# Performance work log

Hardware: AMD Instinct MI355X
Metric: run time of the kernel (lower is better)

The kernel has to match this reference:

```python
import jax, jax.numpy as jnp
import numpy as np

DIM = 1024
HEADS = 16
DH = DIM // HEADS  # 64
DFF = 4096
EPS = 1e-5


def layer_norm(x, g, b):
    mu = jnp.mean(x, axis=-1, keepdims=True)
    var = jnp.mean(jnp.square(x - mu), axis=-1, keepdims=True)
    return (x - mu) * jax.lax.rsqrt(var + EPS) * g + b


def setup_inputs() -> dict:
    key = jax.random.key(0)
    ks = jax.random.split(key, 12)
    s = 0.02
    return {
        "encoder_input": jax.random.normal(ks[0], (4, 2048, DIM), jnp.float32),
        # per-head Q/K/V projections stacked over heads: [H, dim, d_head]
        "wq": jax.random.normal(ks[1], (HEADS, DIM, DH), jnp.float32) * s,
        "bq": jnp.zeros((HEADS, DH), jnp.float32),
        "wk": jax.random.normal(ks[2], (HEADS, DIM, DH), jnp.float32) * s,
        "bk": jnp.zeros((HEADS, DH), jnp.float32),
        "wv": jax.random.normal(ks[3], (HEADS, DIM, DH), jnp.float32) * s,
        "bv": jnp.zeros((HEADS, DH), jnp.float32),
        "ln1_g": jnp.ones((DIM,), jnp.float32),
        "ln1_b": jnp.zeros((DIM,), jnp.float32),
        "w1": jax.random.normal(ks[4], (DIM, DFF), jnp.float32) * s,
        "b1": jnp.zeros((DFF,), jnp.float32),
        "w2": jax.random.normal(ks[5], (DFF, DIM), jnp.float32) * s,
        "b2": jnp.zeros((DIM,), jnp.float32),
        "ln2_g": jnp.ones((DIM,), jnp.float32),
        "ln2_b": jnp.zeros((DIM,), jnp.float32),
    }


def reference(encoder_input, wq, bq, wk, bk, wv, bv, ln1_g, ln1_b,
              w1, b1, w2, b2, ln2_g, ln2_b):
    x = encoder_input  # [B, S, D]
    B, S, D = x.shape
    # per-head projections, batched over heads (same math as the head loop)
    q = jnp.einsum('bsd,hde->bhse', x, wq) + bq[None, :, None, :]
    k = jnp.einsum('bsd,hde->bhse', x, wk) + bk[None, :, None, :]
    v = jnp.einsum('bsd,hde->bhse', x, wv) + bv[None, :, None, :]
    scores = jnp.einsum('bhse,bhte->bhst', q, k) / jnp.sqrt(jnp.float32(DH))
    attn = jax.nn.softmax(scores, axis=-1)
    o = jnp.einsum('bhst,bhte->bhse', attn, v)  # [B, H, S, dh]
    self_attn = jnp.transpose(o, (0, 2, 1, 3)).reshape(B, S, D)  # concat heads on dim=2
    # residual: source + LayerNorm(target)  (dropout = identity in eval)
    res1 = x + layer_norm(self_attn, ln1_g, ln1_b)
    ff = jax.nn.relu(res1 @ w1 + b1) @ w2 + b2
    return res1 + layer_norm(ff, ln2_g, ln2_b)
```

## Files before the change

kernel.cpp:

```cpp
#include <hip/hip_runtime.h>
#include <cstdint>
#include <cmath>

typedef unsigned short u16;
using bf16x8 = __attribute__((ext_vector_type(8))) __bf16;
using f32x4  = __attribute__((ext_vector_type(4))) float;

#define MFMA(a, b, c) __builtin_amdgcn_mfma_f32_16x16x32_bf16((a), (b), (c), 0, 0, 0)

__device__ __forceinline__ float b2f(u16 u) {
    union { unsigned int i; float f; } x; x.i = ((unsigned int)u) << 16; return x.f;
}
__device__ __forceinline__ u16 f2b(float f) {
    union { float f; unsigned int i; } x; x.f = f;
    unsigned int r = x.i + 0x7FFFu + ((x.i >> 16) & 1u);
    return (u16)(r >> 16);
}
__device__ __forceinline__ u16 cvtb(float f) {
    __bf16 h = (__bf16)f;
    return *reinterpret_cast<u16*>(&h);
}
__device__ __forceinline__ uint32_t cvtpk(float lo, float hi) {
    uint32_t r;
    asm("v_cvt_pk_bf16_f32 %0, %1, %2" : "=v"(r) : "v"(lo), "v"(hi));
    return r;
}

__device__ __forceinline__ void gload16(const u16* g, u16* l) {
    __builtin_amdgcn_global_load_lds(
        (const __attribute__((address_space(1))) void*)g,
        (__attribute__((address_space(3))) void*)l, 16, 0, 0);
}

#define BAR do { asm volatile("" ::: "memory"); \
                 __builtin_amdgcn_s_barrier();  \
                 asm volatile("" ::: "memory"); } while (0)

#define QSCALE (0.125f * 1.44269504f)

__global__ __launch_bounds__(256) void xcvt_kernel(const float* __restrict__ X,
                                                   u16* __restrict__ Xb)
{
    size_t i = ((size_t)blockIdx.x * 256 + threadIdx.x) * 8;
    float4 a = *reinterpret_cast<const float4*>(&X[i]);
    float4 b = *reinterpret_cast<const float4*>(&X[i + 4]);
    ushort4 lo = {f2b(a.x), f2b(a.y), f2b(a.z), f2b(a.w)};
    ushort4 hi = {f2b(b.x), f2b(b.y), f2b(b.z), f2b(b.w)};
    *reinterpret_cast<ushort4*>(&Xb[i]) = lo;
    *reinterpret_cast<ushort4*>(&Xb[i + 4]) = hi;
}

__global__ __launch_bounds__(256) void wT_kernel(const float* __restrict__ W,
                                                 u16* __restrict__ Wt, int K, int N)
{
    __shared__ __align__(16) u16 Ts[64][72];
    const int k0 = blockIdx.x * 64, n0 = blockIdx.y * 64;
    const int tid = threadIdx.x;
    #pragma unroll
    for (int it = 0; it < 4; ++it) {
        int vI = tid + it * 256;
        int kr = vI >> 4, nc = (vI & 15) * 4;
        float4 f = *reinterpret_cast<const float4*>(&W[(size_t)(k0 + kr) * N + n0 + nc]);
        Ts[nc + 0][kr] = f2b(f.x);
        Ts[nc + 1][kr] = f2b(f.y);
        Ts[nc + 2][kr] = f2b(f.z);
        Ts[nc + 3][kr] = f2b(f.w);
    }
    __syncthreads();
    #pragma unroll
    for (int it = 0; it < 2; ++it) {
        int vI = tid + it * 256;
        int nr = vI >> 3, kc = (vI & 7) * 8;
        *reinterpret_cast<uint4*>(&Wt[(size_t)(n0 + nr) * K + k0 + kc]) =
            *reinterpret_cast<uint4*>(&Ts[nr][kc]);
    }
}

__global__ __launch_bounds__(256) void wqkvT_kernel(
    const float* __restrict__ Wq, const float* __restrict__ Wk,
    const float* __restrict__ Wv, u16* __restrict__ Wt)
{
    __shared__ __align__(16) u16 Ts[64][72];
    const int k0 = blockIdx.x * 64, h = blockIdx.y, m = blockIdx.z;
    const float* W = (m == 0 ? Wq : (m == 1 ? Wk : Wv)) + (size_t)h * 65536;
    const float scl = (m == 0) ? QSCALE : 1.0f;
    const int tid = threadIdx.x;
    #pragma unroll
    for (int it = 0; it < 4; ++it) {
        int vI = tid + it * 256;
        int kr = vI >> 4, dc = (vI & 15) * 4;
        float4 f = *reinterpret_cast<const float4*>(&W[(size_t)(k0 + kr) * 64 + dc]);
        Ts[dc + 0][kr] = f2b(f.x * scl);
        Ts[dc + 1][kr] = f2b(f.y * scl);
        Ts[dc + 2][kr] = f2b(f.z * scl);
        Ts[dc + 3][kr] = f2b(f.w * scl);
    }
    __syncthreads();
    #pragma unroll
    for (int it = 0; it < 2; ++it) {
        int vI = tid + it * 256;
        int dr = vI >> 3, kc = (vI & 7) * 8;
        *reinterpret_cast<uint4*>(
            &Wt[((size_t)(m * 1024 + h * 64 + dr)) * 1024 + k0 + kc]) =
            *reinterpret_cast<uint4*>(&Ts[dr][kc]);
    }
}

__global__ __launch_bounds__(256) void biascat_kernel(
    const float* __restrict__ Bq, const float* __restrict__ Bk,
    const float* __restrict__ Bv, float* __restrict__ out)
{
    int i = blockIdx.x * 256 + threadIdx.x;
    const float* B = (i < 1024 ? Bq : (i < 2048 ? Bk : Bv));
    float v = B[i & 1023];
    if (i < 1024) v *= QSCALE;
    out[i] = v;
}

__device__ __forceinline__ void stage_half(const u16* __restrict__ gb, int K,
                                           u16* lr, int lane, int w)
{
    #pragma unroll
    for (int cc = 0; cc < 2; ++cc) {
        int c = w * 2 + cc;
        int l = c * 64 + lane;
        int lp = l ^ ((l >> 3) & 7);
        gload16(gb + (size_t)(lp >> 3) * K + (lp & 7) * 8, lr + c * 512);
    }
}

template <int RELU, int F32OUT>
__global__ __launch_bounds__(512, 2) void gemm8(
    const u16* __restrict__ A, const u16* __restrict__ Bt,
    const float* __restrict__ bias, void* __restrict__ Cv,
    int M, int N, int K)
{
    __shared__ __align__(16) u16 lds[65536];
    const int tid = threadIdx.x, lane = tid & 63, w = tid >> 6;
    const int wm = w >> 2, wn = w & 3;
    const int g = lane >> 4, ln = lane & 15;
    const int xr = (ln & 7) << 3;
    const int brow = (wn & 1) * 64;

    int nwg = gridDim.x * gridDim.y;
    int bid = blockIdx.y * gridDim.x + blockIdx.x;
    int swz = (bid & 7) * (nwg >> 3) + (bid >> 3);
    const int m0 = (swz % gridDim.x) * 256;
    const int n0 = (swz / gridDim.x) * 256;

    const u16* Ab = A + (size_t)m0 * K;
    const u16* Bb = Bt + (size_t)n0 * K;

    u16* ldsA[2] = { lds + wm * 8192,         lds + 32768 + wm * 8192 };
    u16* ldsB[2] = { lds + 16384 + (wn >> 1) * 8192,
                     lds + 49152 + (wn >> 1) * 8192 };

    f32x4 acc[8][4];
    #pragma unroll
    for (int i = 0; i < 8; ++i)
        #pragma unroll
        for (int j = 0; j < 4; ++j) acc[i][j] = (f32x4){0.f, 0.f, 0.f, 0.f};

    bf16x8 af[4][2], bf[2][2];

#define RD_A(d, mh)                                                           \
    _Pragma("unroll") for (int i = 0; i < 4; ++i)                             \
    _Pragma("unroll") for (int kk = 0; kk < 2; ++kk)                          \
        af[i][kk] = *(const bf16x8*)&ldsA[d][((mh)*64 + i*16 + ln)*64 +       \
                                             ((kk*32 + g*8) ^ xr)];
#define RD_B(d, nh)                                                           \
    _Pragma("unroll") for (int j = 0; j < 2; ++j)                             \
    _Pragma("unroll") for (int kk = 0; kk < 2; ++kk)                          \
        bf[j][kk] = *(const bf16x8*)&ldsB[d][(brow + (nh)*32 + j*16 + ln)*64  \
                                             + ((kk*32 + g*8) ^ xr)];
#define MMQ(mh, nh)                                                           \
    __builtin_amdgcn_s_setprio(1);                                            \
    _Pragma("unroll") for (int i = 0; i < 4; ++i)                             \
    _Pragma("unroll") for (int j = 0; j < 2; ++j) {                           \
        acc[(mh)*4+i][(nh)*2+j] =                                             \
            MFMA(af[i][0], bf[j][0], acc[(mh)*4+i][(nh)*2+j]);                \
        acc[(mh)*4+i][(nh)*2+j] =                                             \
            MFMA(af[i][1], bf[j][1], acc[(mh)*4+i][(nh)*2+j]);                \
    }                                                                         \
    __builtin_amdgcn_s_setprio(0);

    const int ntk = K >> 6;
    const int nit = ntk >> 1;

    stage_half(Ab,                           K, lds + 0,     lane, w);
    stage_half(Ab + (size_t)128 * K,         K, lds + 8192,  lane, w);
    stage_half(Bb,                           K, lds + 16384, lane, w);
    stage_half(Bb + (size_t)128 * K,         K, lds + 24576, lane, w);
    stage_half(Ab + 64,                      K, lds + 32768, lane, w);
    stage_half(Ab + (size_t)128 * K + 64,    K, lds + 40960, lane, w);
    asm volatile("s_waitcnt vmcnt(4)" ::: "memory");
    BAR;

    for (int u = 0; u < nit; ++u) {
        const int t1 = 2 * u + 1;
        int s0 = 2 * u + 2; if (s0 >= ntk) s0 = ntk - 1;
        int s1 = 2 * u + 3; if (s1 >= ntk) s1 = ntk - 1;
        RD_A(0, 0); RD_B(0, 0);
        stage_half(Bb + (size_t)t1 * 64, K, lds + 49152, lane, w);
        BAR; MMQ(0, 0); BAR;
        RD_B(0, 1);
        stage_half(Bb + (size_t)128 * K + (size_t)t1 * 64, K, lds + 57344, lane, w);
        BAR; MMQ(0, 1); BAR;
        RD_A(0, 1); RD_B(0, 0);
        BAR; MMQ(1, 0); BAR;
        RD_B(0, 1);
        stage_half(Ab + (size_t)s0 * 64, K, lds + 0, lane, w);
        BAR; MMQ(1, 1);
        asm volatile("s_waitcnt vmcnt(2)" ::: "memory");
        BAR;
        RD_A(1, 0); RD_B(1, 0);
        stage_half(Ab + (size_t)128 * K + (size_t)s0 * 64, K, lds + 8192, lane, w);
        BAR; MMQ(0, 0); BAR;
        RD_B(1, 1);
        stage_half(Bb + (size_t)s0 * 64, K, lds + 16384, lane, w);
        BAR; MMQ(0, 1); BAR;
        RD_A(1, 1); RD_B(1, 0);
        stage_half(Bb + (size_t)128 * K + (size_t)s0 * 64, K, lds + 24576, lane, w);
        BAR; MMQ(1, 0); BAR;
        RD_B(1, 1);
        stage_half(Ab + (size_t)s1 * 64, K, lds + 32768, lane, w);
        stage_half(Ab + (size_t)128 * K + (size_t)s1 * 64, K, lds + 40960, lane, w);
        BAR; MMQ(1, 1);
        asm volatile("s_waitcnt vmcnt(4)" ::: "memory");
        BAR;
    }
#undef RD_A
#undef RD_B
#undef MMQ

    asm volatile("s_waitcnt vmcnt(0)" ::: "memory");
    BAR;

    if (F32OUT) {
        float* C = (float*)Cv;
        float bv[4];
        #pragma unroll
        for (int j = 0; j < 4; ++j) bv[j] = bias[n0 + wn * 64 + j * 16 + ln];
        #pragma unroll
        for (int i = 0; i < 8; ++i)
            #pragma unroll
            for (int j = 0; j < 4; ++j)
                #pragma unroll
                for (int r = 0; r < 4; ++r) {
                    float v = acc[i][j][r] + bv[j];
                    if (RELU) v = fmaxf(v, 0.f);
                    int row = m0 + wm * 128 + i * 16 + g * 4 + r;
                    int col = n0 + wn * 64 + j * 16 + ln;
                    C[(size_t)row * N + col] = v;
                }
    } else {
        u16* C = (u16*)Cv;
        float bv[4];
        #pragma unroll
        for (int j = 0; j < 4; ++j) bv[j] = bias[n0 + wn * 64 + j * 16 + ln];
        #pragma unroll
        for (int i = 0; i < 8; ++i)
            #pragma unroll
            for (int j = 0; j < 4; ++j)
                #pragma unroll
                for (int r = 0; r < 4; ++r) {
                    float v = acc[i][j][r] + bv[j];
                    if (RELU) v = fmaxf(v, 0.f);
                    int row = wm * 128 + i * 16 + g * 4 + r;
                    int col = wn * 64 + j * 16 + ln;
                    lds[row * 256 + (col ^ ((row & 12) << 2))] = cvtb(v);
                }
        BAR;
        #pragma unroll
        for (int p = 0; p < 16; ++p) {
            int f = (p * 512 + tid) * 8;
            int row = f >> 8, col = f & 255;
            uint4 val = *(uint4*)&lds[row * 256 + (col ^ ((row & 12) << 2))];
            *(uint4*)&C[(size_t)(m0 + row) * N + n0 + col] = val;
        }
    }
}

template <int RELU, int F32OUT>
__global__ __launch_bounds__(512, 2) void gemm3(
    const u16* __restrict__ A, const u16* __restrict__ Bt,
    const float* __restrict__ bias, void* __restrict__ Cv,
    int M, int N, int K)
{
    __shared__ __align__(16) u16 lds[73728];
    const int tid = threadIdx.x, lane = tid & 63, w = tid >> 6;
    const int wm = w >> 2, wn = w & 3;
    const int g = lane >> 4, ln = lane & 15;
    const int xr = (ln & 7) << 3;
    const int bro = (wn & 1) * 64;

    int nwg = gridDim.x * gridDim.y;
    int bid = blockIdx.y * gridDim.x + blockIdx.x;
    int swz = (bid & 7) * (nwg >> 3) + (bid >> 3);
    const int m0 = (swz % gridDim.x) * 128;
    const int n0 = (swz / gridDim.x) * 256;

    const u16* Ab = A + (size_t)m0 * K;
    const u16* Bb = Bt + (size_t)n0 * K;

    f32x4 acc[4][4];
    #pragma unroll
    for (int i = 0; i < 4; ++i)
        #pragma unroll
        for (int j = 0; j < 4; ++j) acc[i][j] = (f32x4){0.f, 0.f, 0.f, 0.f};

    const int ntk = K >> 6;

    #pragma unroll
    for (int u = 0; u < 2; ++u) {
        stage_half(Ab + (size_t)u * 64, K, lds + u * 24576, lane, w);
        stage_half(Bb + (size_t)u * 64, K, lds + u * 24576 + 8192, lane, w);
        stage_half(Bb + (size_t)128 * K + (size_t)u * 64, K,
                   lds + u * 24576 + 16384, lane, w);
    }

    bf16x8 af[4][2], bf[2][2];

    for (int u = 0; u < ntk; ++u) {
        const int p = u % 3;
        if (u < ntk - 1) asm volatile("s_waitcnt vmcnt(6)" ::: "memory");
        else             asm volatile("s_waitcnt vmcnt(0)" ::: "memory");
        BAR;
        u16* bufA = lds + p * 24576;
        u16* bufB = lds + p * 24576 + 8192 + (wn >> 1) * 8192;
        const int us = u + 2;
        const int ps = us % 3;
        #pragma unroll
        for (int i = 0; i < 4; ++i)
            #pragma unroll
            for (int kk = 0; kk < 2; ++kk)
                af[i][kk] = *(const bf16x8*)&bufA[(wm * 64 + i * 16 + ln) * 64 +
                                                 ((kk * 32 + g * 8) ^ xr)];
        #pragma unroll
        for (int j = 0; j < 2; ++j)
            #pragma unroll
            for (int kk = 0; kk < 2; ++kk)
                bf[j][kk] = *(const bf16x8*)&bufB[(bro + j * 16 + ln) * 64 +
                                                  ((kk * 32 + g * 8) ^ xr)];
        if (us < ntk)
            stage_half(Ab + (size_t)us * 64, K, lds + ps * 24576, lane, w);
        __builtin_amdgcn_s_setprio(1);
        #pragma unroll
        for (int i = 0; i < 4; ++i)
            #pragma unroll
            for (int j = 0; j < 2; ++j) {
                acc[i][j] = MFMA(af[i][0], bf[j][0], acc[i][j]);
                acc[i][j] = MFMA(af[i][1], bf[j][1], acc[i][j]);
            }
        __builtin_amdgcn_s_setprio(0);
        #pragma unroll
        for (int j = 0; j < 2; ++j)
            #pragma unroll
            for (int kk = 0; kk < 2; ++kk)
                bf[j][kk] = *(const bf16x8*)&bufB[(bro + 32 + j * 16 + ln) * 64 +
                                                  ((kk * 32 + g * 8) ^ xr)];
        if (us < ntk) {
            stage_half(Bb + (size_t)us * 64, K, lds + ps * 24576 + 8192, lane, w);
            stage_half(Bb + (size_t)128 * K + (size_t)us * 64, K,
                       lds + ps * 24576 + 16384, lane, w);
        }
        __builtin_amdgcn_s_setprio(1);
        #pragma unroll
        for (int i = 0; i < 4; ++i)
            #pragma unroll
            for (int j = 0; j < 2; ++j) {
                acc[i][2 + j] = MFMA(af[i][0], bf[j][0], acc[i][2 + j]);
                acc[i][2 + j] = MFMA(af[i][1], bf[j][1], acc[i][2 + j]);
            }
        __builtin_amdgcn_s_setprio(0);
    }

    float bv[4];
    #pragma unroll
    for (int j = 0; j < 4; ++j) bv[j] = bias[n0 + wn * 64 + j * 16 + ln];

    if (F32OUT) {
        float* C = (float*)Cv;
        #pragma unroll
        for (int i = 0; i < 4; ++i)
            #pragma unroll
            for (int j = 0; j < 4; ++j)
                #pragma unroll
                for (int r = 0; r < 4; ++r) {
                    float v = acc[i][j][r] + bv[j];
                    if (RELU) v = fmaxf(v, 0.f);
                    int row = m0 + wm * 64 + i * 16 + g * 4 + r;
                    int col = n0 + wn * 64 + j * 16 + ln;
                    C[(size_t)row * N + col] = v;
                }
    } else {
        u16* C = (u16*)Cv;
        BAR;
        #pragma unroll
        for (int i = 0; i < 4; ++i)
            #pragma unroll
            for (int j = 0; j < 4; ++j)
                #pragma unroll
                for (int r = 0; r < 4; ++r) {
                    float v = acc[i][j][r] + bv[j];
                    if (RELU) v = fmaxf(v, 0.f);
                    int row = wm * 64 + i * 16 + g * 4 + r;
                    int col = wn * 64 + j * 16 + ln;
                    lds[row * 256 + (col ^ ((row & 12) << 2))] = cvtb(v);
                }
        BAR;
        #pragma unroll
        for (int p2 = 0; p2 < 8; ++p2) {
            int f = (p2 * 512 + tid) * 8;
            int row = f >> 8, col = f & 255;
            uint4 val = *(uint4*)&lds[row * 256 + (col ^ ((row & 12) << 2))];
            *(uint4*)&C[(size_t)(m0 + row) * N + n0 + col] = val;
        }
    }
}

__device__ __forceinline__ int sperm(int row) {
    return (row & 32) | ((row & 12) << 1) | ((row & 16) >> 2) | (row & 3);
}

__global__ __launch_bounds__(512, 4) void attn_kernel(
    const u16* __restrict__ QKV, u16* __restrict__ O)
{
    const int bh = blockIdx.x, b = bh >> 4, h = bh & 15;
    const int q0 = blockIdx.y * 256;
    const int tid = threadIdx.x;
    const int lane = tid & 63, w = tid >> 6;
    const int g = lane >> 4, ln = lane & 15;

    __shared__ __align__(16) u16 Ks[2][64][72];
    __shared__ __align__(16) u16 Vt2[2][64][72];

    const u16* Qp = QKV + (size_t)b * 2048 * 3072 + h * 64;
    const u16* Kp = Qp + 1024;
    const u16* Vp = Qp + 2048;

    bf16x8 qf[2][2];
    #pragma unroll
    for (int i = 0; i < 2; ++i)
        #pragma unroll
        for (int kk = 0; kk < 2; ++kk)
            qf[i][kk] = *reinterpret_cast<const bf16x8*>(
                &Qp[(size_t)(q0 + w * 32 + i * 16 + ln) * 3072 + kk * 32 + g * 8]);

    f32x4 oacc[2][4], oext[2];
    #pragma unroll
    for (int i = 0; i < 2; ++i) {
        #pragma unroll
        for (int n = 0; n < 4; ++n) oacc[i][n] = (f32x4){0.f, 0.f, 0.f, 0.f};
        oext[i] = (f32x4){0.f, 0.f, 0.f, 0.f};
    }

    bf16x8 onesv;
    #pragma unroll
    for (int z = 0; z < 8; ++z) onesv[z] = (__bf16)1.0f;

    const int r0 = tid >> 3, c0 = (tid & 7) * 8;
    const int ss0 = sperm(r0) ^ c0;

    {
        uint4 ka = *reinterpret_cast<const uint4*>(&Kp[(size_t)r0 * 3072 + c0]);
        uint4 va = *reinterpret_cast<const uint4*>(&Vp[(size_t)r0 * 3072 + c0]);
        *reinterpret_cast<uint4*>(&Ks[0][r0][c0]) = ka;
        const u16* tva = reinterpret_cast<const u16*>(&va);
        #pragma unroll
        for (int j = 0; j < 8; ++j) Vt2[0][c0 + j][ss0] = tva[j];
    }
    __syncthreads();

    for (int t = 0; t < 32; ++t) {
        const int c = t & 1;
        uint4 ka, va;
        if (t < 31) {
            const size_t rb0 = (size_t)((t + 1) * 64 + r0) * 3072 + c0;
            ka = *reinterpret_cast<const uint4*>(&Kp[rb0]);
            va = *reinterpret_cast<const uint4*>(&Vp[rb0]);
        }

        f32x4 sc[4][2];
        #pragma unroll
        for (int j = 0; j < 4; ++j)
            #pragma unroll
            for (int i = 0; i < 2; ++i) sc[j][i] = (f32x4){0.f, 0.f, 0.f, 0.f};
        #pragma unroll
        for (int kk = 0; kk < 2; ++kk)
            #pragma unroll
            for (int j = 0; j < 4; ++j) {
                bf16x8 kf = *(const bf16x8*)&Ks[c][j * 16 + ln][kk * 32 + g * 8];
                sc[j][0] = MFMA(kf, qf[0][kk], sc[j][0]);
                sc[j][1] = MFMA(kf, qf[1][kk], sc[j][1]);
            }

        uint32_t pk[2][8];
        #pragma unroll
        for (int i = 0; i < 2; ++i)
            #pragma unroll
            for (int j = 0; j < 4; ++j) {
                #pragma unroll
                for (int r = 0; r < 4; ++r)
                    sc[j][i][r] = exp2f(sc[j][i][r]);
                pk[i][j * 2 + 0] = cvtpk(sc[j][i][0], sc[j][i][1]);
                pk[i][j * 2 + 1] = cvtpk(sc[j][i][2], sc[j][i][3]);
            }

        #pragma unroll
        for (int kk = 0; kk < 2; ++kk) {
            union { uint32_t u[4]; bf16x8 v; } a0, a1;
            a0.u[0] = pk[0][kk * 4 + 0]; a0.u[1] = pk[0][kk * 4 + 1];
            a0.u[2] = pk[0][kk * 4 + 2]; a0.u[3] = pk[0][kk * 4 + 3];
            a1.u[0] = pk[1][kk * 4 + 0]; a1.u[1] = pk[1][kk * 4 + 1];
            a1.u[2] = pk[1][kk * 4 + 2]; a1.u[3] = pk[1][kk * 4 + 3];
            #pragma unroll
            for (int n = 0; n < 4; ++n) {
                int d = n * 16 + ln;
                bf16x8 vf = *(const bf16x8*)&Vt2[c][d][(kk * 32 + g * 8) ^ (d & 56)];
                oacc[0][n] = MFMA(a0.v, vf, oacc[0][n]);
                oacc[1][n] = MFMA(a1.v, vf, oacc[1][n]);
            }
            oext[0] = MFMA(a0.v, onesv, oext[0]);
            oext[1] = MFMA(a1.v, onesv, oext[1]);
        }

        if (t < 31) {
            *reinterpret_cast<uint4*>(&Ks[c ^ 1][r0][c0]) = ka;
            const u16* tva = reinterpret_cast<const u16*>(&va);
            #pragma unroll
            for (int j = 0; j < 8; ++j) Vt2[c ^ 1][c0 + j][ss0] = tva[j];
        }
        __syncthreads();
    }

    #pragma unroll
    for (int i = 0; i < 2; ++i)
        #pragma unroll
        for (int r = 0; r < 4; ++r) {
            float rv = __builtin_amdgcn_rcpf(oext[i][r]);
            int row = q0 + w * 32 + i * 16 + g * 4 + r;
            #pragma unroll
            for (int n = 0; n < 4; ++n)
                O[((size_t)(b * 2048 + row)) * 1024 + h * 64 + n * 16 + ln] =
                    cvtb(oacc[i][n][r] * rv);
        }
}

template <int T_F32, int SRC_F32, int OUT_F32>
__global__ __launch_bounds__(256) void ln_add_kernel(
    const void* __restrict__ TV, const void* __restrict__ SrcV,
    const float* __restrict__ G, const float* __restrict__ Bt,
    void* __restrict__ OutV)
{
    const int row = blockIdx.x;
    const int tid = threadIdx.x;
    __shared__ float red[8];

    const size_t rb = (size_t)row * 1024;
    float v0, v1, v2, v3;
    if (T_F32) {
        float4 tv = *reinterpret_cast<const float4*>((const float*)TV + rb + tid * 4);
        v0 = tv.x; v1 = tv.y; v2 = tv.z; v3 = tv.w;
    } else {
        ushort4 tv = *reinterpret_cast<const ushort4*>((const u16*)TV + rb + tid * 4);
        v0 = b2f(tv.x); v1 = b2f(tv.y); v2 = b2f(tv.z); v3 = b2f(tv.w);
    }
    float s = v0 + v1 + v2 + v3;
    float sq = v0 * v0 + v1 * v1 + v2 * v2 + v3 * v3;
    #pragma unroll
    for (int mm = 1; mm < 64; mm <<= 1) {
        s += __shfl_xor(s, mm);
        sq += __shfl_xor(sq, mm);
    }
    if ((tid & 63) == 0) { red[tid >> 6] = s; red[4 + (tid >> 6)] = sq; }
    __syncthreads();
    s = red[0] + red[1] + red[2] + red[3];
    sq = red[4] + red[5] + red[6] + red[7];
    float mu = s * (1.f / 1024.f);
    float var = sq * (1.f / 1024.f) - mu * mu;
    float rs = rsqrtf(var + 1e-5f);

    float s0, s1, s2, s3;
    if (SRC_F32) {
        float4 sv = *reinterpret_cast<const float4*>((const float*)SrcV + rb + tid * 4);
        s0 = sv.x; s1 = sv.y; s2 = sv.z; s3 = sv.w;
    } else {
        ushort4 sv = *reinterpret_cast<const ushort4*>((const u16*)SrcV + rb + tid * 4);
        s0 = b2f(sv.x); s1 = b2f(sv.y); s2 = b2f(sv.z); s3 = b2f(sv.w);
    }
    float4 gv = *reinterpret_cast<const float4*>(&G[tid * 4]);
    float4 bv = *reinterpret_cast<const float4*>(&Bt[tid * 4]);
    float o0 = s0 + (v0 - mu) * rs * gv.x + bv.x;
    float o1 = s1 + (v1 - mu) * rs * gv.y + bv.y;
    float o2 = s2 + (v2 - mu) * rs * gv.z + bv.z;
    float o3 = s3 + (v3 - mu) * rs * gv.w + bv.w;
    if (OUT_F32) {
        float4 ov = {o0, o1, o2, o3};
        *reinterpret_cast<float4*>((float*)OutV + rb + tid * 4) = ov;
    } else {
        ushort4 ov = {f2b(o0), f2b(o1), f2b(o2), f2b(o3)};
        *reinterpret_cast<ushort4*>((u16*)OutV + rb + tid * 4) = ov;
    }
}

extern "C" void kernel_launch(void* const* d_in, const int* in_sizes, int n_in,
                              void* d_out, int out_size, void* d_ws, size_t ws_size,
                              hipStream_t stream)
{
    const float* X   = (const float*)d_in[0];
    const float* Wq  = (const float*)d_in[1];
    const float* Bq  = (const float*)d_in[2];
    const float* Wk  = (const float*)d_in[3];
    const float* Bk  = (const float*)d_in[4];
    const float* Wv  = (const float*)d_in[5];
    const float* Bv  = (const float*)d_in[6];
    const float* g1  = (const float*)d_in[7];
    const float* b1  = (const float*)d_in[8];
    const float* W1  = (const float*)d_in[9];
    const float* B1  = (const float*)d_in[10];
    const float* W2  = (const float*)d_in[11];
    const float* B2  = (const float*)d_in[12];
    const float* g2  = (const float*)d_in[13];
    const float* b2  = (const float*)d_in[14];
    float* out = (float*)d_out;

    char* ws = (char*)d_ws;
    const size_t MiB = 1048576;
    u16*   qkv   = (u16*)(ws);
    u16*   Xb    = (u16*)(ws + 48 * MiB);
    u16*   attnb = (u16*)(ws + 48 * MiB);
    u16*   wqkvt = (u16*)(ws + 64 * MiB);
    float* bcat  = (float*)(ws + 70 * MiB);
    u16*   res1  = (u16*)(ws + 64 * MiB);
    u16*   hid   = (u16*)(ws);
    u16*   w1t   = (u16*)(ws + 80 * MiB);
    u16*   w2t   = (u16*)(ws + 88 * MiB);

    xcvt_kernel<<<4096, 256, 0, stream>>>(X, Xb);
    wT_kernel<<<dim3(16, 64), 256, 0, stream>>>(W1, w1t, 1024, 4096);
    wT_kernel<<<dim3(64, 16), 256, 0, stream>>>(W2, w2t, 4096, 1024);
    wqkvT_kernel<<<dim3(16, 16, 3), 256, 0, stream>>>(Wq, Wk, Wv, wqkvt);
    biascat_kernel<<<12, 256, 0, stream>>>(Bq, Bk, Bv, bcat);

    gemm3<0, 0><<<dim3(64, 12), 512, 0, stream>>>(Xb, wqkvt, bcat, qkv, 8192, 3072, 1024);
    attn_kernel<<<dim3(64, 8), 512, 0, stream>>>(qkv, attnb);
    ln_add_kernel<0, 1, 0><<<8192, 256, 0, stream>>>(attnb, X, g1, b1, res1);

    gemm8<1, 0><<<dim3(32, 16), 512, 0, stream>>>(res1, w1t, B1, hid, 8192, 4096, 1024);
    gemm3<0, 1><<<dim3(64, 4), 512, 0, stream>>>(hid, w2t, B2, out, 8192, 1024, 4096);
    ln_add_kernel<1, 0, 1><<<8192, 256, 0, stream>>>(out, res1, g2, b2, out);
}
```

Measured before the change: 331.4 us.

## Split attention KV range in two and fuse partial combine into LN1

The attention kernel gets a second grid dimension so each block handles half of the key/value sequence. It writes unnormalized bf16 partial outputs and fp32 row sums to separate buffers. A new LN1 kernel adds the two partials, normalizes by the combined sum, and applies the residual layer norm. The weight-transpose launches move after attention because the new partial buffers reuse that workspace. The aim is to double the number of attention blocks for better CU occupancy, at the cost of extra partial-buffer traffic and some bf16 rounding of unnormalized sums.

```diff
diff --git a/kernel.cpp b/kernel.cpp
--- a/kernel.cpp
+++ b/kernel.cpp
@@ -424,10 +424,11 @@
 }
 
 __global__ __launch_bounds__(512, 4) void attn_kernel(
-    const u16* __restrict__ QKV, u16* __restrict__ O)
+    const u16* __restrict__ QKV, u16* __restrict__ pO, float* __restrict__ pL)
 {
     const int bh = blockIdx.x, b = bh >> 4, h = bh & 15;
     const int q0 = blockIdx.y * 256;
+    const int half = blockIdx.z;
     const int tid = threadIdx.x;
     const int lane = tid & 63, w = tid >> 6;
     const int g = lane >> 4, ln = lane & 15;
@@ -436,8 +437,8 @@
     __shared__ __align__(16) u16 Vt2[2][64][72];
 
     const u16* Qp = QKV + (size_t)b * 2048 * 3072 + h * 64;
-    const u16* Kp = Qp + 1024;
-    const u16* Vp = Qp + 2048;
+    const u16* Kp = Qp + 1024 + (size_t)half * 1024 * 3072;
+    const u16* Vp = Qp + 2048 + (size_t)half * 1024 * 3072;
 
     bf16x8 qf[2][2];
     #pragma unroll
@@ -472,10 +473,10 @@
     }
     __syncthreads();
 
-    for (int t = 0; t < 32; ++t) {
+    for (int t = 0; t < 16; ++t) {
         const int c = t & 1;
         uint4 ka, va;
-        if (t < 31) {
+        if (t < 15) {
             const size_t rb0 = (size_t)((t + 1) * 64 + r0) * 3072 + c0;
             ka = *reinterpret_cast<const uint4*>(&Kp[rb0]);
             va = *reinterpret_cast<const uint4*>(&Vp[rb0]);
@@ -525,7 +526,7 @@
             oext[1] = MFMA(a1.v, onesv, oext[1]);
         }
 
-        if (t < 31) {
+        if (t < 15) {
             *reinterpret_cast<uint4*>(&Ks[c ^ 1][r0][c0]) = ka;
             const u16* tva = reinterpret_cast<const u16*>(&va);
             #pragma unroll
@@ -534,17 +535,77 @@
         __syncthreads();
     }
 
+    u16* pOh = pO + (size_t)half * 8192 * 1024;
     #pragma unroll
     for (int i = 0; i < 2; ++i)
         #pragma unroll
         for (int r = 0; r < 4; ++r) {
-            float rv = __builtin_amdgcn_rcpf(oext[i][r]);
             int row = q0 + w * 32 + i * 16 + g * 4 + r;
             #pragma unroll
             for (int n = 0; n < 4; ++n)
-                O[((size_t)(b * 2048 + row)) * 1024 + h * 64 + n * 16 + ln] =
-                    cvtb(oacc[i][n][r] * rv);
+                pOh[((size_t)(b * 2048 + row)) * 1024 + h * 64 + n * 16 + ln] =
+                    cvtb(oacc[i][n][r]);
         }
+    if (ln == 0) {
+        #pragma unroll
+        for (int i = 0; i < 2; ++i)
+            #pragma unroll
+            for (int r = 0; r < 4; ++r) {
+                int row = q0 + w * 32 + i * 16 + g * 4 + r;
+                pL[(size_t)half * 131072 + ((size_t)(b * 16 + h)) * 2048 + row] =
+                    oext[i][r];
+            }
+    }
+}
+
+__global__ __launch_bounds__(256) void ln1_comb_kernel(
+    const u16* __restrict__ P0, const u16* __restrict__ P1,
+    const float* __restrict__ PL, const float* __restrict__ X,
+    const float* __restrict__ G, const float* __restrict__ Bt,
+    u16* __restrict__ Out)
+{
+    const int row = blockIdx.x;
+    const int tid = threadIdx.x;
+    const int b = row >> 11, s = row & 2047;
+    const int h = tid >> 4;
+    __shared__ float red[8];
+
+    const size_t rb = (size_t)row * 1024;
+    const size_t pli = ((size_t)(b * 16 + h)) * 2048 + s;
+    float l = PL[pli] + PL[131072 + pli];
+    float rv = __builtin_amdgcn_rcpf(l);
+
+    ushort4 a0 = *reinterpret_cast<const ushort4*>(&P0[rb + tid * 4]);
+    ushort4 a1 = *reinterpret_cast<const ushort4*>(&P1[rb + tid * 4]);
+    float v0 = (b2f(a0.x) + b2f(a1.x)) * rv;
+    float v1 = (b2f(a0.y) + b2f(a1.y)) * rv;
+    float v2 = (b2f(a0.z) + b2f(a1.z)) * rv;
+    float v3 = (b2f(a0.w) + b2f(a1.w)) * rv;
+
+    float sm = v0 + v1 + v2 + v3;
+    float sq = v0 * v0 + v1 * v1 + v2 * v2 + v3 * v3;
+    #pragma unroll
+    for (int mm = 1; mm < 64; mm <<= 1) {
+        sm += __shfl_xor(sm, mm);
+        sq += __shfl_xor(sq, mm);
+    }
+    if ((tid & 63) == 0) { red[tid >> 6] = sm; red[4 + (tid >> 6)] = sq; }
+    __syncthreads();
+    sm = red[0] + red[1] + red[2] + red[3];
+    sq = red[4] + red[5] + red[6] + red[7];
+    float mu = sm * (1.f / 1024.f);
+    float var = sq * (1.f / 1024.f) - mu * mu;
+    float rs = rsqrtf(var + 1e-5f);
+
+    float4 sv = *reinterpret_cast<const float4*>(&X[rb + tid * 4]);
+    float4 gv = *reinterpret_cast<const float4*>(&G[tid * 4]);
+    float4 bv = *reinterpret_cast<const float4*>(&Bt[tid * 4]);
+    ushort4 ov;
+    ov.x = f2b(sv.x + (v0 - mu) * rs * gv.x + bv.x);
+    ov.y = f2b(sv.y + (v1 - mu) * rs * gv.y + bv.y);
+    ov.z = f2b(sv.z + (v2 - mu) * rs * gv.z + bv.z);
+    ov.w = f2b(sv.w + (v3 - mu) * rs * gv.w + bv.w);
+    *reinterpret_cast<ushort4*>(&Out[rb + tid * 4]) = ov;
 }
 
 template <int T_F32, int SRC_F32, int OUT_F32>
@@ -629,7 +690,9 @@
     const size_t MiB = 1048576;
     u16*   qkv   = (u16*)(ws);
     u16*   Xb    = (u16*)(ws + 48 * MiB);
-    u16*   attnb = (u16*)(ws + 48 * MiB);
+    u16*   p0    = (u16*)(ws + 48 * MiB);
+    u16*   p1    = (u16*)(ws + 64 * MiB);
+    float* pL    = (float*)(ws + 80 * MiB);
     u16*   wqkvt = (u16*)(ws + 64 * MiB);
     float* bcat  = (float*)(ws + 70 * MiB);
     u16*   res1  = (u16*)(ws + 64 * MiB);
@@ -638,14 +701,15 @@
     u16*   w2t   = (u16*)(ws + 88 * MiB);
 
     xcvt_kernel<<<4096, 256, 0, stream>>>(X, Xb);
+    wqkvT_kernel<<<dim3(16, 16, 3), 256, 0, stream>>>(Wq, Wk, Wv, wqkvt);
+    biascat_kernel<<<12, 256, 0, stream>>>(Bq, Bk, Bv, bcat);
+
+    gemm3<0, 0><<<dim3(64, 12), 512, 0, stream>>>(Xb, wqkvt, bcat, qkv, 8192, 3072, 1024);
+    attn_kernel<<<dim3(64, 8, 2), 512, 0, stream>>>(qkv, p0, pL);
+    ln1_comb_kernel<<<8192, 256, 0, stream>>>(p0, p1, pL, X, g1, b1, res1);
+
     wT_kernel<<<dim3(16, 64), 256, 0, stream>>>(W1, w1t, 1024, 4096);
     wT_kernel<<<dim3(64, 16), 256, 0, stream>>>(W2, w2t, 4096, 1024);
-    wqkvT_kernel<<<dim3(16, 16, 3), 256, 0, stream>>>(Wq, Wk, Wv, wqkvt);
-    biascat_kernel<<<12, 256, 0, stream>>>(Bq, Bk, Bv, bcat);
-
-    gemm3<0, 0><<<dim3(64, 12), 512, 0, stream>>>(Xb, wqkvt, bcat, qkv, 8192, 3072, 1024);
-    attn_kernel<<<dim3(64, 8), 512, 0, stream>>>(qkv, attnb);
-    ln_add_kernel<0, 1, 0><<<8192, 256, 0, stream>>>(attnb, X, g1, b1, res1);
 
     gemm8<1, 0><<<dim3(32, 16), 512, 0, stream>>>(res1, w1t, B1, hid, 8192, 4096, 1024);
     gemm3<0, 1><<<dim3(64, 4), 512, 0, stream>>>(hid, w2t, B2, out, 8192, 1024, 4096);
```

After: 335.9 us. No clear change (+1.4%).
